# Kernel tuning notes

Hardware: AMD Instinct MI355X
Metric: run time of the kernel (lower is better)

Reference implementation:

```python
import jax, jax.numpy as jnp
import numpy as np
import math

B, C, DH = 2048, 64, 512
CAP_VOCAB = 11  # max(core_capacities)+1
DIST_VOCAB = 3


def setup_inputs() -> dict:
    key = jax.random.key(0)
    ks = jax.random.split(key, 12)
    inp = {
        "Ht_C": jax.random.normal(ks[0], (B, C, DH), jnp.float32),
        "core_capacities": jax.random.randint(ks[1], (B, C), 0, CAP_VOCAB),
        "distances": jax.random.randint(ks[2], (B, C), 0, DIST_VOCAB),
        "H_X": jax.random.normal(ks[3], (B, DH), jnp.float32),
        "Ht_S": jax.random.normal(ks[4], (B, DH), jnp.float32),
        "Eq_Q": jax.random.normal(ks[5], (B, DH), jnp.float32),
        "double": jax.random.randint(ks[6], (B,), 0, 2).astype(bool),
        # learned parameters (nn.Embedding tables and bias-free Linear weights, [out,in])
        "cap_emb": jax.random.normal(ks[7], (CAP_VOCAB, DH), jnp.float32) * 0.02,
        "dist_emb": jax.random.normal(ks[8], (DIST_VOCAB, DH), jnp.float32) * 0.02,
        "W_q": jax.random.normal(ks[9], (DH, 3 * DH), jnp.float32) * (1.0 / math.sqrt(3 * DH)),
        "W_k": jax.random.normal(ks[10], (DH, DH), jnp.float32) * (1.0 / math.sqrt(DH)),
        "W_v": jax.random.normal(ks[11], (DH, DH), jnp.float32) * (1.0 / math.sqrt(DH)),
    }
    return inp


def reference(Ht_C, core_capacities, distances, H_X, Ht_S, Eq_Q, double,
              cap_emb, dist_emb, W_q, W_k, W_v):
    scale = 1.0 / math.sqrt(Ht_C.shape[-1])  # 1/sqrt(d_H), slice_emb_size == d_H
    # dynamic core embeddings G_{t,q}^{(C)}: [B,C,dH]
    G = Ht_C + cap_emb[core_capacities] + dist_emb[distances]
    # context and projections
    context = jnp.concatenate([H_X, Ht_S, Eq_Q], axis=-1)          # [B,3dH]
    Q = context @ W_q.T                                            # [B,dH]
    K = jnp.einsum('bcd,ed->bce', G, W_k)                          # [B,C,dH]
    V = jnp.einsum('bcd,ed->bce', G, W_v)                          # [B,C,dH]
    # glimpse attention over cores
    attn_logits = jnp.einsum('bcd,bd->bc', K, Q) * scale           # [B,C]
    attn_weights = jax.nn.softmax(attn_logits, axis=-1)            # softmax over cores
    glimpse = jnp.einsum('bc,bcd->bd', attn_weights, V)            # [B,dH]
    # pointer logits + capacity mask
    u = jnp.einsum('bcd,bd->bc', K, glimpse) * scale               # [B,C]
    need = jnp.where(double[:, None], 2, 1)                        # [B,1]
    invalid = core_capacities < need                               # [B,C]
    u = jnp.where(invalid, -jnp.inf, u)
    return jax.nn.softmax(u, axis=-1)                              # [B,C]
```

## Files before the change

### kernel.cpp

```cpp
#include <hip/hip_runtime.h>
#include <math.h>

#define DH 512
#define CC 64
#define NB 2048
#define SCALE 0.044194173824159216f

__device__ __forceinline__ float wsum(float v) {
#pragma unroll
  for (int off = 32; off; off >>= 1) v += __shfl_xor(v, off, 64);
  return v;
}

__global__ __launch_bounds__(128) void pre_kernel(const float* __restrict__ Wq,
                                                  const float* __restrict__ Wv,
                                                  const float* __restrict__ Wk,
                                                  float* __restrict__ Aout,
                                                  float* __restrict__ Mout,
                                                  const unsigned char* __restrict__ dbl,
                                                  int* __restrict__ need) {
  const int bx = blockIdx.x;
  const int t = threadIdx.x;
  if (bx == 256) {
    __shared__ int flagNZ, flagFP;
    if (t == 0) { flagNZ = 0; flagFP = 0; }
    __syncthreads();
    int nz = 0, fp = 0;
    for (int i = t; i < NB; i += 128) {
      if (i & 3) {
        unsigned char v = dbl[i];
        nz |= (v != 0);
        fp |= (v == 0x3f) | (v == 0x80);
      }
    }
    if (nz) atomicOr(&flagNZ, 1);
    if (fp) atomicOr(&flagFP, 1);
    __syncthreads();
    const int isFP = flagFP, isByte = flagNZ && !flagFP;
    for (int i = t; i < NB; i += 128) {
      int v;
      if (isFP)        v = (((const float*)dbl)[i] != 0.0f);
      else if (isByte) v = (dbl[i] != 0);
      else             v = (((const int*)dbl)[i] != 0);
      need[i] = v ? 2 : 1;
    }
    return;
  }
  __shared__ float As[16][64];
  __shared__ float Bs[16][64];
  const int mt = bx >> 3, nt = bx & 7;
  const int m0 = mt * 64, n0 = nt * 64;
  const bool isQ = (m0 < 1536);
  const float* Acol = isQ ? (Wq + m0) : (Wv + (m0 - 1536));
  const int lda = isQ ? 1536 : 512;
  float* Cout = isQ ? (Aout + (size_t)m0 * 512) : (Mout + (size_t)(m0 - 1536) * 512);
  const int lr = t >> 3;
  const int lc = (t & 7) << 3;
  const int tx = t & 15, ty = t >> 4;

  float4 ra0, ra1, rb0, rb1;
  ra0 = *(const float4*)&Acol[(size_t)lr * lda + lc];
  ra1 = *(const float4*)&Acol[(size_t)lr * lda + lc + 4];
  rb0 = *(const float4*)&Wk[(size_t)lr * 512 + n0 + lc];
  rb1 = *(const float4*)&Wk[(size_t)lr * 512 + n0 + lc + 4];
  float acc[8][4] = {};
  for (int k0 = 0; k0 < 512; k0 += 16) {
    __syncthreads();
    *(float4*)&As[lr][lc] = ra0;
    *(float4*)&As[lr][lc + 4] = ra1;
    *(float4*)&Bs[lr][lc] = rb0;
    *(float4*)&Bs[lr][lc + 4] = rb1;
    __syncthreads();
    if (k0 + 16 < 512) {
      const int kn = k0 + 16 + lr;
      ra0 = *(const float4*)&Acol[(size_t)kn * lda + lc];
      ra1 = *(const float4*)&Acol[(size_t)kn * lda + lc + 4];
      rb0 = *(const float4*)&Wk[(size_t)kn * 512 + n0 + lc];
      rb1 = *(const float4*)&Wk[(size_t)kn * 512 + n0 + lc + 4];
    }
#pragma unroll
    for (int k = 0; k < 16; ++k) {
      float4 a0 = *(float4*)&As[k][ty << 3];
      float4 a1 = *(float4*)&As[k][(ty << 3) + 4];
      float4 b  = *(float4*)&Bs[k][tx << 2];
      float av[8] = {a0.x, a0.y, a0.z, a0.w, a1.x, a1.y, a1.z, a1.w};
      float bv[4] = {b.x, b.y, b.z, b.w};
#pragma unroll
      for (int i = 0; i < 8; ++i)
#pragma unroll
        for (int j = 0; j < 4; ++j) acc[i][j] = fmaf(av[i], bv[j], acc[i][j]);
    }
  }
#pragma unroll
  for (int i = 0; i < 8; ++i) {
    float4 o = {acc[i][0], acc[i][1], acc[i][2], acc[i][3]};
    *(float4*)&Cout[(size_t)((ty << 3) + i) * 512 + n0 + (tx << 2)] = o;
  }
}

#define AS_STR 132

__global__ __launch_bounds__(256) void gemm_nn2p(const float* __restrict__ A0,
                                                 const float* __restrict__ A1,
                                                 const float* __restrict__ A2,
                                                 const float* __restrict__ B,
                                                 float* __restrict__ Cp,
                                                 int kchunk) {
  __shared__ float As[16 * AS_STR];
  __shared__ float Bs[16 * 64];
  const int t = threadIdx.x;
  const int m0 = blockIdx.x * 128, n0 = blockIdx.y * 64;
  const int kbeg = blockIdx.z * kchunk, kend = kbeg + kchunk;
  float* C = Cp + (size_t)blockIdx.z * (NB * DH);
  const int tx = t & 15, ty = t >> 4;
  const int ar0 = t >> 2;
  const int ak4 = (t & 3) << 2;
  const int bk = t >> 4, bn4 = (t & 15) << 2;

  float4 ra0, ra1, rb;
  {
    const float* base = (kbeg < 512) ? A0 : ((kbeg < 1024) ? A1 : A2);
    const int kk = kbeg & 511;
    ra0 = *(const float4*)&base[(size_t)(m0 + ar0) * 512 + kk + ak4];
    ra1 = *(const float4*)&base[(size_t)(m0 + ar0 + 64) * 512 + kk + ak4];
    rb  = *(const float4*)&B[(size_t)(kbeg + bk) * 512 + n0 + bn4];
  }
  float acc[8][4] = {};
  for (int k0 = kbeg; k0 < kend; k0 += 16) {
    __syncthreads();
    As[(ak4 + 0) * AS_STR + ar0] = ra0.x;
    As[(ak4 + 1) * AS_STR + ar0] = ra0.y;
    As[(ak4 + 2) * AS_STR + ar0] = ra0.z;
    As[(ak4 + 3) * AS_STR + ar0] = ra0.w;
    As[(ak4 + 0) * AS_STR + ar0 + 64] = ra1.x;
    As[(ak4 + 1) * AS_STR + ar0 + 64] = ra1.y;
    As[(ak4 + 2) * AS_STR + ar0 + 64] = ra1.z;
    As[(ak4 + 3) * AS_STR + ar0 + 64] = ra1.w;
    *(float4*)&Bs[bk * 64 + bn4] = rb;
    __syncthreads();
    if (k0 + 16 < kend) {
      const int kn = k0 + 16;
      const float* base = (kn < 512) ? A0 : ((kn < 1024) ? A1 : A2);
      const int kk = kn & 511;
      ra0 = *(const float4*)&base[(size_t)(m0 + ar0) * 512 + kk + ak4];
      ra1 = *(const float4*)&base[(size_t)(m0 + ar0 + 64) * 512 + kk + ak4];
      rb  = *(const float4*)&B[(size_t)(kn + bk) * 512 + n0 + bn4];
    }
#pragma unroll
    for (int k = 0; k < 16; ++k) {
      float4 a0 = *(float4*)&As[k * AS_STR + (ty << 3)];
      float4 a1 = *(float4*)&As[k * AS_STR + (ty << 3) + 4];
      float4 b  = *(float4*)&Bs[k * 64 + (tx << 2)];
      float av[8] = {a0.x, a0.y, a0.z, a0.w, a1.x, a1.y, a1.z, a1.w};
      float bv[4] = {b.x, b.y, b.z, b.w};
#pragma unroll
      for (int i = 0; i < 8; ++i)
#pragma unroll
        for (int j = 0; j < 4; ++j) acc[i][j] = fmaf(av[i], bv[j], acc[i][j]);
    }
  }
#pragma unroll
  for (int i = 0; i < 8; ++i) {
    float4 o = {acc[i][0], acc[i][1], acc[i][2], acc[i][3]};
    *(float4*)&C[(size_t)(m0 + (ty << 3) + i) * 512 + n0 + (tx << 2)] = o;
  }
}

__global__ __launch_bounds__(256, 4) void fused_kernel(const float* __restrict__ HtC,
                                                       const int* __restrict__ caps,
                                                       const int* __restrict__ dists,
                                                       const float* __restrict__ Qkp,
                                                       const float* __restrict__ Mm,
                                                       const float* __restrict__ cap_emb,
                                                       const float* __restrict__ dist_emb,
                                                       const int* __restrict__ need,
                                                       float* __restrict__ out) {
  const int t = threadIdx.x;
  const int wv = t >> 6, ln = t & 63;
  const int b0 = blockIdx.x << 1;

  __shared__ float qk[2][DH];
  __shared__ float Gws[2][DH];
  __shared__ float gks[2][DH];
  __shared__ float gkp[2][2][DH];
  __shared__ float accs[4][DH];
  __shared__ float ec[CC];
  __shared__ float capQ[2][11], distQ[2][3];
  __shared__ float capE[11], distE[3];
  __shared__ float capG[2][11], distG[2][3];
  __shared__ float lsum_s;
  __shared__ int capsS[2][CC], distsS[2][CC];

  if (t < 128) {
    int hh = t >> 6, c = t & 63;
    capsS[hh][c] = caps[(size_t)(b0 + hh) * CC + c];
    distsS[hh][c] = dists[(size_t)(b0 + hh) * CC + c];
  }

#pragma unroll
  for (int h = 0; h < 2; ++h) {
    const size_t bo = (size_t)(b0 + h) * DH;
    float q0 = 0.f, q1 = 0.f;
#pragma unroll
    for (int z = 0; z < 4; ++z) {
      q0 += Qkp[(size_t)z * NB * DH + bo + t];
      q1 += Qkp[(size_t)z * NB * DH + bo + 256 + t];
    }
    qk[h][t] = q0;
    qk[h][t + 256] = q1;
  }
  __syncthreads();

#pragma unroll
  for (int h = 0; h < 2; ++h) {
#pragma unroll
    for (int r = 0; r < 3; ++r) {
      int v = wv + (r << 2);
      if (v < 11) {
        float s = 0.f;
#pragma unroll
        for (int j = 0; j < 8; ++j) s = fmaf(cap_emb[v * DH + ln + (j << 6)], qk[h][ln + (j << 6)], s);
        s = wsum(s);
        if (ln == 0) capQ[h][v] = s;
      }
    }
    if (wv < 3) {
      float s = 0.f;
#pragma unroll
      for (int j = 0; j < 8; ++j) s = fmaf(dist_emb[wv * DH + ln + (j << 6)], qk[h][ln + (j << 6)], s);
      s = wsum(s);
      if (ln == 0) distQ[h][wv] = s;
    }
  }

  for (int h = 0; h < 2; ++h) {
    const int b = b0 + h;
    if (t < 11) capE[t] = 0.f;
    if (t < 3) distE[t] = 0.f;
    __syncthreads();
    const float4* qk4 = (const float4*)qk[h];
    float4 q1 = qk4[ln];
    float4 q2 = qk4[64 + ln];
    const float* hb = HtC + (size_t)b * CC * DH;

    float sp[16];
#pragma unroll
    for (int g = 0; g < 2; ++g) {
#pragma unroll
      for (int i = 0; i < 8; ++i) {
        const int c = (wv << 4) + (g << 3) + i;
        const float4* h4 = (const float4*)(hb + (size_t)c * DH);
        float4 h1 = h4[ln];
        float4 h2 = h4[64 + ln];
        sp[(g << 3) + i] = h1.x * q1.x + h1.y * q1.y + h1.z * q1.z + h1.w * q1.w +
                           h2.x * q2.x + h2.y * q2.y + h2.z * q2.z + h2.w * q2.w;
      }
    }
#pragma unroll
    for (int i = 0; i < 16; ++i) sp[i] = wsum(sp[i]);
    float ei[16];
#pragma unroll
    for (int i = 0; i < 16; ++i) {
      int c = (wv << 4) + i;
      float logit = SCALE * (sp[i] + capQ[h][capsS[h][c]] + distQ[h][distsS[h][c]]);
      ei[i] = __expf(logit);
    }
    if (ln == 0) {
#pragma unroll
      for (int i = 0; i < 16; ++i) ec[(wv << 4) + i] = ei[i];
    }
    float a0 = 0.f, a1 = 0.f, a2 = 0.f, a3 = 0.f, a4 = 0.f, a5 = 0.f, a6 = 0.f, a7 = 0.f;
#pragma unroll
    for (int i = 0; i < 16; ++i) {
      const float4* h4 = (const float4*)(hb + (size_t)((wv << 4) + i) * DH);
      float4 h1 = h4[ln];
      float4 h2 = h4[64 + ln];
      a0 = fmaf(ei[i], h1.x, a0); a1 = fmaf(ei[i], h1.y, a1);
      a2 = fmaf(ei[i], h1.z, a2); a3 = fmaf(ei[i], h1.w, a3);
      a4 = fmaf(ei[i], h2.x, a4); a5 = fmaf(ei[i], h2.y, a5);
      a6 = fmaf(ei[i], h2.z, a6); a7 = fmaf(ei[i], h2.w, a7);
    }
    {
      int d0 = ln << 2;
      accs[wv][d0 + 0] = a0; accs[wv][d0 + 1] = a1;
      accs[wv][d0 + 2] = a2; accs[wv][d0 + 3] = a3;
      accs[wv][256 + d0 + 0] = a4; accs[wv][256 + d0 + 1] = a5;
      accs[wv][256 + d0 + 2] = a6; accs[wv][256 + d0 + 3] = a7;
    }
    __syncthreads();
    if (t < CC) {
      float e = ec[t];
      float l = wsum(e);
      if (t == 0) lsum_s = l;
      atomicAdd(&capE[capsS[h][t]], e);
      atomicAdd(&distE[distsS[h][t]], e);
    }
    __syncthreads();
    const float rinv = 1.0f / lsum_s;
#pragma unroll
    for (int dd = 0; dd < 2; ++dd) {
      int d = t + (dd << 8);
      float g = accs[0][d] + accs[1][d] + accs[2][d] + accs[3][d];
#pragma unroll
      for (int v = 0; v < 11; ++v) g = fmaf(capE[v], cap_emb[v * DH + d], g);
#pragma unroll
      for (int v = 0; v < 3; ++v) g = fmaf(distE[v], dist_emb[v * DH + d], g);
      Gws[h][d] = g * rinv;
    }
    __syncthreads();
  }

  {
    const int e4 = (t & 127) << 2;
    const int half = t >> 7;
    const float* Mp = Mm + (size_t)(half << 8) * DH + e4;
    const float* g0p = &Gws[0][half << 8];
    const float* g1p = &Gws[1][half << 8];
    float s00 = 0.f, s01 = 0.f, s02 = 0.f, s03 = 0.f;
    float s10 = 0.f, s11 = 0.f, s12 = 0.f, s13 = 0.f;
#pragma unroll 8
    for (int d = 0; d < 256; ++d) {
      float4 m4 = *(const float4*)&Mp[(size_t)d * DH];
      float g0 = g0p[d];
      float g1 = g1p[d];
      s00 = fmaf(g0, m4.x, s00); s01 = fmaf(g0, m4.y, s01);
      s02 = fmaf(g0, m4.z, s02); s03 = fmaf(g0, m4.w, s03);
      s10 = fmaf(g1, m4.x, s10); s11 = fmaf(g1, m4.y, s11);
      s12 = fmaf(g1, m4.z, s12); s13 = fmaf(g1, m4.w, s13);
    }
    gkp[half][0][e4 + 0] = s00; gkp[half][0][e4 + 1] = s01;
    gkp[half][0][e4 + 2] = s02; gkp[half][0][e4 + 3] = s03;
    gkp[half][1][e4 + 0] = s10; gkp[half][1][e4 + 1] = s11;
    gkp[half][1][e4 + 2] = s12; gkp[half][1][e4 + 3] = s13;
  }
  __syncthreads();
#pragma unroll
  for (int h = 0; h < 2; ++h) {
    gks[h][t] = gkp[0][h][t] + gkp[1][h][t];
    gks[h][t + 256] = gkp[0][h][t + 256] + gkp[1][h][t + 256];
  }
  __syncthreads();

#pragma unroll
  for (int h = 0; h < 2; ++h) {
#pragma unroll
    for (int r = 0; r < 3; ++r) {
      int v = wv + (r << 2);
      if (v < 11) {
        float s = 0.f;
#pragma unroll
        for (int j = 0; j < 8; ++j) s = fmaf(cap_emb[v * DH + ln + (j << 6)], gks[h][ln + (j << 6)], s);
        s = wsum(s);
        if (ln == 0) capG[h][v] = s;
      }
    }
    if (wv < 3) {
      float s = 0.f;
#pragma unroll
      for (int j = 0; j < 8; ++j) s = fmaf(dist_emb[wv * DH + ln + (j << 6)], gks[h][ln + (j << 6)], s);
      s = wsum(s);
      if (ln == 0) distG[h][wv] = s;
    }
  }
  __syncthreads();

  for (int h = 1; h >= 0; --h) {
    const int b = b0 + h;
    const float4* gk4 = (const float4*)gks[h];
    float4 q1 = gk4[ln];
    float4 q2 = gk4[64 + ln];
    const float* hb = HtC + (size_t)b * CC * DH;
    float sp[16];
#pragma unroll
    for (int g = 0; g < 2; ++g) {
#pragma unroll
      for (int i = 0; i < 8; ++i) {
        const int c = (wv << 4) + (g << 3) + i;
        const float4* h4 = (const float4*)(hb + (size_t)c * DH);
        float4 h1 = h4[ln];
        float4 h2 = h4[64 + ln];
        sp[(g << 3) + i] = h1.x * q1.x + h1.y * q1.y + h1.z * q1.z + h1.w * q1.w +
                           h2.x * q2.x + h2.y * q2.y + h2.z * q2.z + h2.w * q2.w;
      }
    }
#pragma unroll
    for (int i = 0; i < 16; ++i) sp[i] = wsum(sp[i]);
    if (ln == 0) {
#pragma unroll
      for (int i = 0; i < 16; ++i) {
        int c = (wv << 4) + i;
        ec[c] = SCALE * (sp[i] + capG[h][capsS[h][c]] + distG[h][distsS[h][c]]);
      }
    }
    __syncthreads();
    if (t < CC) {
      int nb = need[b];
      float x = ec[t];
      if (capsS[h][t] < nb) x = -INFINITY;
      float m = x;
#pragma unroll
      for (int off = 32; off; off >>= 1) m = fmaxf(m, __shfl_xor(m, off, 64));
      float e = __expf(x - m);
      float ssum = wsum(e);
      out[(size_t)b * CC + t] = e / ssum;
    }
    __syncthreads();
  }
}

extern "C" void kernel_launch(void* const* d_in, const int* in_sizes, int n_in,
                              void* d_out, int out_size, void* d_ws, size_t ws_size,
                              hipStream_t stream) {
  const float* HtC      = (const float*)d_in[0];
  const int* caps       = (const int*)d_in[1];
  const int* dists      = (const int*)d_in[2];
  const float* H_X      = (const float*)d_in[3];
  const float* Ht_S     = (const float*)d_in[4];
  const float* Eq_Q     = (const float*)d_in[5];
  const unsigned char* dbl = (const unsigned char*)d_in[6];
  const float* cap_emb  = (const float*)d_in[7];
  const float* dist_emb = (const float*)d_in[8];
  const float* W_q      = (const float*)d_in[9];
  const float* W_k      = (const float*)d_in[10];
  const float* W_v      = (const float*)d_in[11];
  float* out = (float*)d_out;

  float* ws     = (float*)d_ws;
  float* wsA    = ws;
  float* wsM    = wsA + 1536 * 512;
  float* wsQkp  = wsM + 512 * 512;
  int* wsNeed   = (int*)(wsQkp + 4 * 2048 * 512);

  pre_kernel<<<257, 128, 0, stream>>>(W_q, W_v, W_k, wsA, wsM, dbl, wsNeed);
  gemm_nn2p<<<dim3(16, 8, 4), 256, 0, stream>>>(H_X, Ht_S, Eq_Q, wsA, wsQkp, 384);
  fused_kernel<<<NB / 2, 256, 0, stream>>>(HtC, caps, dists, wsQkp, wsM,
                                           cap_emb, dist_emb, wsNeed, out);
}
```

Measured before the change: 578.7 us.

## Restructure core scoring loops so each thread owns a contiguous 32-element slice

The per-core dot products and weighted accumulation now assign each 16-lane group one core and each lane a contiguous 32-float slice, instead of every wave reducing over all 64 lanes for each of 16 cores. This replaces the 16 full-wave shuffle reductions with 4-step partial reductions, and lets a single load of H feed both the dot product and the exp-weighted accumulation, avoiding the second read of HtC. Shared buffers are padded (36-float stride per 32 elements) to avoid LDS bank conflicts on the new float4 access pattern. The cost is more registers for the 8-float4 accumulators and a serial k loop with less memory-level parallelism.

```diff
diff --git a/kernel.cpp b/kernel.cpp
--- a/kernel.cpp
+++ b/kernel.cpp
@@ -5,6 +5,8 @@
 #define CC 64
 #define NB 2048
 #define SCALE 0.044194173824159216f
+
+#define PD(d) ((((d) >> 5) * 36) + ((d) & 31))
 
 __device__ __forceinline__ float wsum(float v) {
 #pragma unroll
@@ -177,13 +179,14 @@
                                                        float* __restrict__ out) {
   const int t = threadIdx.x;
   const int wv = t >> 6, ln = t & 63;
+  const int g = ln >> 4, l16 = ln & 15;
   const int b0 = blockIdx.x << 1;
 
-  __shared__ float qk[2][DH];
+  __shared__ float qk[2][576];
+  __shared__ float gks[2][576];
+  __shared__ float accs[4][576];
   __shared__ float Gws[2][DH];
-  __shared__ float gks[2][DH];
   __shared__ float gkp[2][2][DH];
-  __shared__ float accs[4][DH];
   __shared__ float ec[CC];
   __shared__ float capQ[2][11], distQ[2][3];
   __shared__ float capE[11], distE[3];
@@ -206,8 +209,8 @@
       q0 += Qkp[(size_t)z * NB * DH + bo + t];
       q1 += Qkp[(size_t)z * NB * DH + bo + 256 + t];
     }
-    qk[h][t] = q0;
-    qk[h][t + 256] = q1;
+    qk[h][PD(t)] = q0;
+    qk[h][PD(t + 256)] = q1;
   }
   __syncthreads();
 
@@ -219,7 +222,8 @@
       if (v < 11) {
         float s = 0.f;
 #pragma unroll
-        for (int j = 0; j < 8; ++j) s = fmaf(cap_emb[v * DH + ln + (j << 6)], qk[h][ln + (j << 6)], s);
+        for (int j = 0; j < 8; ++j)
+          s = fmaf(cap_emb[v * DH + ln + (j << 6)], qk[h][PD(ln + (j << 6))], s);
         s = wsum(s);
         if (ln == 0) capQ[h][v] = s;
       }
@@ -227,7 +231,8 @@
     if (wv < 3) {
       float s = 0.f;
 #pragma unroll
-      for (int j = 0; j < 8; ++j) s = fmaf(dist_emb[wv * DH + ln + (j << 6)], qk[h][ln + (j << 6)], s);
+      for (int j = 0; j < 8; ++j)
+        s = fmaf(dist_emb[wv * DH + ln + (j << 6)], qk[h][PD(ln + (j << 6))], s);
       s = wsum(s);
       if (ln == 0) distQ[h][wv] = s;
     }
@@ -238,54 +243,49 @@
     if (t < 11) capE[t] = 0.f;
     if (t < 3) distE[t] = 0.f;
     __syncthreads();
-    const float4* qk4 = (const float4*)qk[h];
-    float4 q1 = qk4[ln];
-    float4 q2 = qk4[64 + ln];
+    float4 qs[8];
+#pragma unroll
+    for (int j = 0; j < 8; ++j) qs[j] = *(const float4*)&qk[h][l16 * 36 + 4 * j];
+    float4 ac[8];
+#pragma unroll
+    for (int j = 0; j < 8; ++j) ac[j] = make_float4(0.f, 0.f, 0.f, 0.f);
     const float* hb = HtC + (size_t)b * CC * DH;
-
-    float sp[16];
-#pragma unroll
-    for (int g = 0; g < 2; ++g) {
-#pragma unroll
-      for (int i = 0; i < 8; ++i) {
-        const int c = (wv << 4) + (g << 3) + i;
-        const float4* h4 = (const float4*)(hb + (size_t)c * DH);
-        float4 h1 = h4[ln];
-        float4 h2 = h4[64 + ln];
-        sp[(g << 3) + i] = h1.x * q1.x + h1.y * q1.y + h1.z * q1.z + h1.w * q1.w +
-                           h2.x * q2.x + h2.y * q2.y + h2.z * q2.z + h2.w * q2.w;
-      }
-    }
-#pragma unroll
-    for (int i = 0; i < 16; ++i) sp[i] = wsum(sp[i]);
-    float ei[16];
-#pragma unroll
-    for (int i = 0; i < 16; ++i) {
-      int c = (wv << 4) + i;
-      float logit = SCALE * (sp[i] + capQ[h][capsS[h][c]] + distQ[h][distsS[h][c]]);
-      ei[i] = __expf(logit);
-    }
-    if (ln == 0) {
-#pragma unroll
-      for (int i = 0; i < 16; ++i) ec[(wv << 4) + i] = ei[i];
-    }
-    float a0 = 0.f, a1 = 0.f, a2 = 0.f, a3 = 0.f, a4 = 0.f, a5 = 0.f, a6 = 0.f, a7 = 0.f;
-#pragma unroll
-    for (int i = 0; i < 16; ++i) {
-      const float4* h4 = (const float4*)(hb + (size_t)((wv << 4) + i) * DH);
-      float4 h1 = h4[ln];
-      float4 h2 = h4[64 + ln];
-      a0 = fmaf(ei[i], h1.x, a0); a1 = fmaf(ei[i], h1.y, a1);
-      a2 = fmaf(ei[i], h1.z, a2); a3 = fmaf(ei[i], h1.w, a3);
-      a4 = fmaf(ei[i], h2.x, a4); a5 = fmaf(ei[i], h2.y, a5);
-      a6 = fmaf(ei[i], h2.z, a6); a7 = fmaf(ei[i], h2.w, a7);
-    }
-    {
-      int d0 = ln << 2;
-      accs[wv][d0 + 0] = a0; accs[wv][d0 + 1] = a1;
-      accs[wv][d0 + 2] = a2; accs[wv][d0 + 3] = a3;
-      accs[wv][256 + d0 + 0] = a4; accs[wv][256 + d0 + 1] = a5;
-      accs[wv][256 + d0 + 2] = a6; accs[wv][256 + d0 + 3] = a7;
+#pragma unroll 1
+    for (int k = 0; k < 4; ++k) {
+      const int c = (wv << 4) + (k << 2) + g;
+      const float* hp = hb + (size_t)c * DH + (l16 << 5);
+      float4 hv[8];
+#pragma unroll
+      for (int j = 0; j < 8; ++j) hv[j] = *(const float4*)&hp[4 * j];
+      float s = 0.f;
+#pragma unroll
+      for (int j = 0; j < 8; ++j) {
+        s = fmaf(hv[j].x, qs[j].x, s); s = fmaf(hv[j].y, qs[j].y, s);
+        s = fmaf(hv[j].z, qs[j].z, s); s = fmaf(hv[j].w, qs[j].w, s);
+      }
+      s += __shfl_xor(s, 1, 64);
+      s += __shfl_xor(s, 2, 64);
+      s += __shfl_xor(s, 4, 64);
+      s += __shfl_xor(s, 8, 64);
+      float e = __expf(SCALE * (s + capQ[h][capsS[h][c]] + distQ[h][distsS[h][c]]));
+      if (l16 == 0) ec[c] = e;
+#pragma unroll
+      for (int j = 0; j < 8; ++j) {
+        ac[j].x = fmaf(e, hv[j].x, ac[j].x); ac[j].y = fmaf(e, hv[j].y, ac[j].y);
+        ac[j].z = fmaf(e, hv[j].z, ac[j].z); ac[j].w = fmaf(e, hv[j].w, ac[j].w);
+      }
+    }
+#pragma unroll
+    for (int j = 0; j < 8; ++j) {
+      ac[j].x += __shfl_xor(ac[j].x, 16, 64); ac[j].x += __shfl_xor(ac[j].x, 32, 64);
+      ac[j].y += __shfl_xor(ac[j].y, 16, 64); ac[j].y += __shfl_xor(ac[j].y, 32, 64);
+      ac[j].z += __shfl_xor(ac[j].z, 16, 64); ac[j].z += __shfl_xor(ac[j].z, 32, 64);
+      ac[j].w += __shfl_xor(ac[j].w, 16, 64); ac[j].w += __shfl_xor(ac[j].w, 32, 64);
+    }
+    if (g == 0) {
+#pragma unroll
+      for (int j = 0; j < 8; ++j)
+        *(float4*)&accs[wv][l16 * 36 + 4 * j] = ac[j];
     }
     __syncthreads();
     if (t < CC) {
@@ -300,12 +300,12 @@
 #pragma unroll
     for (int dd = 0; dd < 2; ++dd) {
       int d = t + (dd << 8);
-      float g = accs[0][d] + accs[1][d] + accs[2][d] + accs[3][d];
-#pragma unroll
-      for (int v = 0; v < 11; ++v) g = fmaf(capE[v], cap_emb[v * DH + d], g);
-#pragma unroll
-      for (int v = 0; v < 3; ++v) g = fmaf(distE[v], dist_emb[v * DH + d], g);
-      Gws[h][d] = g * rinv;
+      float gg = accs[0][PD(d)] + accs[1][PD(d)] + accs[2][PD(d)] + accs[3][PD(d)];
+#pragma unroll
+      for (int v = 0; v < 11; ++v) gg = fmaf(capE[v], cap_emb[v * DH + d], gg);
+#pragma unroll
+      for (int v = 0; v < 3; ++v) gg = fmaf(distE[v], dist_emb[v * DH + d], gg);
+      Gws[h][d] = gg * rinv;
     }
     __syncthreads();
   }
@@ -336,8 +336,8 @@
   __syncthreads();
 #pragma unroll
   for (int h = 0; h < 2; ++h) {
-    gks[h][t] = gkp[0][h][t] + gkp[1][h][t];
-    gks[h][t + 256] = gkp[0][h][t + 256] + gkp[1][h][t + 256];
+    gks[h][PD(t)] = gkp[0][h][t] + gkp[1][h][t];
+    gks[h][PD(t + 256)] = gkp[0][h][t + 256] + gkp[1][h][t + 256];
   }
   __syncthreads();
 
@@ -349,7 +349,8 @@
       if (v < 11) {
         float s = 0.f;
 #pragma unroll
-        for (int j = 0; j < 8; ++j) s = fmaf(cap_emb[v * DH + ln + (j << 6)], gks[h][ln + (j << 6)], s);
+        for (int j = 0; j < 8; ++j)
+          s = fmaf(cap_emb[v * DH + ln + (j << 6)], gks[h][PD(ln + (j << 6))], s);
         s = wsum(s);
         if (ln == 0) capG[h][v] = s;
       }
@@ -357,7 +358,8 @@
     if (wv < 3) {
       float s = 0.f;
 #pragma unroll
-      for (int j = 0; j < 8; ++j) s = fmaf(dist_emb[wv * DH + ln + (j << 6)], gks[h][ln + (j << 6)], s);
+      for (int j = 0; j < 8; ++j)
+        s = fmaf(dist_emb[wv * DH + ln + (j << 6)], gks[h][PD(ln + (j << 6))], s);
       s = wsum(s);
       if (ln == 0) distG[h][wv] = s;
     }
@@ -366,31 +368,29 @@
 
   for (int h = 1; h >= 0; --h) {
     const int b = b0 + h;
-    const float4* gk4 = (const float4*)gks[h];
-    float4 q1 = gk4[ln];
-    float4 q2 = gk4[64 + ln];
+    float4 gs[8];
+#pragma unroll
+    for (int j = 0; j < 8; ++j) gs[j] = *(const float4*)&gks[h][l16 * 36 + 4 * j];
     const float* hb = HtC + (size_t)b * CC * DH;
-    float sp[16];
-#pragma unroll
-    for (int g = 0; g < 2; ++g) {
-#pragma unroll
-      for (int i = 0; i < 8; ++i) {
-        const int c = (wv << 4) + (g << 3) + i;
-        const float4* h4 = (const float4*)(hb + (size_t)c * DH);
-        float4 h1 = h4[ln];
-        float4 h2 = h4[64 + ln];
-        sp[(g << 3) + i] = h1.x * q1.x + h1.y * q1.y + h1.z * q1.z + h1.w * q1.w +
-                           h2.x * q2.x + h2.y * q2.y + h2.z * q2.z + h2.w * q2.w;
-      }
-    }
-#pragma unroll
-    for (int i = 0; i < 16; ++i) sp[i] = wsum(sp[i]);
-    if (ln == 0) {
-#pragma unroll
-      for (int i = 0; i < 16; ++i) {
-        int c = (wv << 4) + i;
-        ec[c] = SCALE * (sp[i] + capG[h][capsS[h][c]] + distG[h][distsS[h][c]]);
-      }
+#pragma unroll 1
+    for (int k = 0; k < 4; ++k) {
+      const int c = (wv << 4) + (k << 2) + g;
+      const float* hp = hb + (size_t)c * DH + (l16 << 5);
+      float4 hv[8];
+#pragma unroll
+      for (int j = 0; j < 8; ++j) hv[j] = *(const float4*)&hp[4 * j];
+      float s = 0.f;
+#pragma unroll
+      for (int j = 0; j < 8; ++j) {
+        s = fmaf(hv[j].x, gs[j].x, s); s = fmaf(hv[j].y, gs[j].y, s);
+        s = fmaf(hv[j].z, gs[j].z, s); s = fmaf(hv[j].w, gs[j].w, s);
+      }
+      s += __shfl_xor(s, 1, 64);
+      s += __shfl_xor(s, 2, 64);
+      s += __shfl_xor(s, 4, 64);
+      s += __shfl_xor(s, 8, 64);
+      if (l16 == 0)
+        ec[c] = SCALE * (s + capG[h][capsS[h][c]] + distG[h][distsS[h][c]]);
     }
     __syncthreads();
     if (t < CC) {
```

New measurement: 553.9 us. 1.04x faster.
